# Performance work log

Hardware: AMD Instinct MI355X
Metric: run time of the kernel (lower is better)

The kernel has to match this reference:

```python
import jax, jax.numpy as jnp
import numpy as np

D_MODEL, N_HEAD, D_HEAD, N_LAYERS, D_FF = 1024, 16, 64, 6, 4096
SEQ_LEN, MEM_LEN, BATCH, CLAMP_LEN = 512, 128, 4, 512
LN_EPS = 1e-5


def layernorm(x, g, b):
    mu = jnp.mean(x, axis=-1, keepdims=True)
    var = jnp.var(x, axis=-1, keepdims=True)
    return (x - mu) * jax.lax.rsqrt(var + LN_EPS) * g + b


def rel_shift(x):
    # x: (qlen, rlen, B, H) -> Transformer-XL relative shift
    q, r, b, n = x.shape
    zp = jnp.zeros((q, 1, b, n), x.dtype)
    xp = jnp.concatenate([zp, x], axis=1).reshape(r + 1, q, b, n)
    return xp[1:].reshape(q, r, b, n)


def pos_embedding(klen):
    # sinusoidal embedding on positions klen-1 .. 0, clamped at CLAMP_LEN
    pos = jnp.arange(klen - 1, -1, -1.0, dtype=jnp.float32)
    pos = jnp.minimum(pos, float(CLAMP_LEN))
    inv_freq = 1.0 / (10000.0 ** (jnp.arange(0.0, D_MODEL, 2.0) / D_MODEL))
    sin_inp = pos[:, None] * inv_freq[None, :]  # (klen, D/2)
    return jnp.concatenate([jnp.sin(sin_inp), jnp.cos(sin_inp)], axis=-1)  # (klen, D)


def setup_inputs() -> dict:
    key = jax.random.key(0)
    ks = jax.random.split(key, 16)
    s = 0.02
    return {
        "inputs": jax.random.normal(ks[0], (SEQ_LEN, BATCH, D_MODEL), jnp.float32),
        "mems": jax.random.normal(ks[1], (N_LAYERS, MEM_LEN, BATCH, D_MODEL), jnp.float32),
        "r_w_bias": jax.random.normal(ks[2], (N_HEAD, D_HEAD), jnp.float32) * s,
        "r_r_bias": jax.random.normal(ks[3], (N_HEAD, D_HEAD), jnp.float32) * s,
        "qkv_w": jax.random.normal(ks[4], (N_LAYERS, 3 * N_HEAD * D_HEAD, D_MODEL), jnp.float32) * s,
        "r_w": jax.random.normal(ks[5], (N_LAYERS, N_HEAD * D_HEAD, D_MODEL), jnp.float32) * s,
        "o_w": jax.random.normal(ks[6], (N_LAYERS, D_MODEL, N_HEAD * D_HEAD), jnp.float32) * s,
        "ln1_g": jnp.ones((N_LAYERS, D_MODEL), jnp.float32),
        "ln1_b": jnp.zeros((N_LAYERS, D_MODEL), jnp.float32),
        "ff_w1": jax.random.normal(ks[7], (N_LAYERS, D_FF, D_MODEL), jnp.float32) * s,
        "ff_b1": jnp.zeros((N_LAYERS, D_FF), jnp.float32),
        "ff_w2": jax.random.normal(ks[8], (N_LAYERS, D_MODEL, D_FF), jnp.float32) * s,
        "ff_b2": jnp.zeros((N_LAYERS, D_MODEL), jnp.float32),
        "ln2_g": jnp.ones((N_LAYERS, D_MODEL), jnp.float32),
        "ln2_b": jnp.zeros((N_LAYERS, D_MODEL), jnp.float32),
        "fin_g": jnp.ones((D_MODEL,), jnp.float32),
        "fin_b": jnp.zeros((D_MODEL,), jnp.float32),
    }


def reference(inputs, mems, r_w_bias, r_r_bias, qkv_w, r_w, o_w,
              ln1_g, ln1_b, ff_w1, ff_b1, ff_w2, ff_b2, ln2_g, ln2_b,
              fin_g, fin_b):
    qlen, bsz, _ = inputs.shape
    mlen = mems.shape[1]
    klen = mlen + qlen
    scale = 1.0 / np.sqrt(D_HEAD)

    pos_emb = pos_embedding(klen)  # (klen, D)
    # causal mask with memory: True = masked
    attn_mask = jnp.triu(jnp.ones((qlen, klen), bool), k=1 + mlen)

    x = inputs  # (T, B, D)
    for l in range(N_LAYERS):
        # ---- relative multi-head attention (pre_lnorm) ----
        cat = jnp.concatenate([mems[l], x], axis=0)           # (klen, B, D)
        h = layernorm(cat, ln1_g[l], ln1_b[l])
        w_heads = jnp.einsum('kbd,ed->kbe', h, qkv_w[l])      # (klen, B, 3HD)
        r_head_k = jnp.einsum('kd,ed->ke', pos_emb, r_w[l])   # (klen, HD)
        hd = N_HEAD * D_HEAD
        q = w_heads[-qlen:, :, :hd].reshape(qlen, bsz, N_HEAD, D_HEAD)
        k = w_heads[:, :, hd:2 * hd].reshape(klen, bsz, N_HEAD, D_HEAD)
        v = w_heads[:, :, 2 * hd:].reshape(klen, bsz, N_HEAD, D_HEAD)
        r_head_k = r_head_k.reshape(klen, N_HEAD, D_HEAD)

        AC = jnp.einsum('ibnd,jbnd->ijbn', q + r_w_bias, k)
        BD = rel_shift(jnp.einsum('ibnd,jnd->ijbn', q + r_r_bias, r_head_k))
        score = (AC + BD) * scale                              # (q, k, B, H)
        score = jnp.where(attn_mask[:, :, None, None], -jnp.inf, score)
        prob = jax.nn.softmax(score, axis=1)
        attn_vec = jnp.einsum('ijbn,jbnd->ibnd', prob, v).reshape(qlen, bsz, hd)
        attn_out = jnp.einsum('ibe,de->ibd', attn_vec, o_w[l])
        x = x + attn_out

        # ---- position-wise FFN (pre_lnorm) ----
        hf = layernorm(x, ln2_g[l], ln2_b[l])
        hf = jax.nn.relu(jnp.einsum('ibd,fd->ibf', hf, ff_w1[l]) + ff_b1[l])
        hf = jnp.einsum('ibf,df->ibd', hf, ff_w2[l]) + ff_b2[l]
        x = x + hf

    return layernorm(x, fin_g, fin_b)
```

## Files before the change

### kernel.cpp

```cpp
#include <hip/hip_runtime.h>
#include <math.h>
#include <stdint.h>

#define DM    1024
#define NH    16
#define DH    64
#define NL    6
#define DFF   4096
#define QLEN  512
#define MLEN  128
#define B_    4
#define KL    640
#define CLAMP 512
#define EPS   1e-5f

typedef _Float16 f16x8 __attribute__((ext_vector_type(8)));
typedef _Float16 f16x4 __attribute__((ext_vector_type(4)));
typedef float    f32x4 __attribute__((ext_vector_type(4)));

__device__ __forceinline__ void gload16(const void* g, void* l) {
  __builtin_amdgcn_global_load_lds(
      (const __attribute__((address_space(1))) void*)g,
      (__attribute__((address_space(3))) void*)l, 16, 0, 0);
}

__device__ __forceinline__ float block_sum(float v, float* sm4) {
#pragma unroll
  for (int o = 32; o > 0; o >>= 1) v += __shfl_down(v, o, 64);
  int lane = threadIdx.x & 63, wid = threadIdx.x >> 6;
  if (lane == 0) sm4[wid] = v;
  __syncthreads();
  float r = sm4[0] + sm4[1] + sm4[2] + sm4[3];
  __syncthreads();
  return r;
}

__global__ __launch_bounds__(256) void pos_emb_kernel(_Float16* __restrict__ pe) {
  int p = blockIdx.x;
  float pos = fminf((float)(KL - 1 - p), (float)CLAMP);
  for (int f = threadIdx.x; f < 512; f += 256) {
    float inv = powf(10000.0f, -(float)f * (1.0f / 512.0f));
    float a = pos * inv;
    pe[(size_t)p * DM + f]       = (_Float16)sinf(a);
    pe[(size_t)p * DM + 512 + f] = (_Float16)cosf(a);
  }
}

__global__ __launch_bounds__(256) void cast_all_kernel(
    const float* __restrict__ qkv, const float* __restrict__ rw,
    const float* __restrict__ ow, const float* __restrict__ f1,
    const float* __restrict__ f2,
    _Float16* __restrict__ dq, _Float16* __restrict__ dr,
    _Float16* __restrict__ dow, _Float16* __restrict__ d1,
    _Float16* __restrict__ d2) {
  size_t i = ((size_t)blockIdx.x * 256 + threadIdx.x) * 8;
  const float* s; _Float16* d; size_t off;
  if (i < 18874368)      { s = qkv; d = dq;  off = 0; }
  else if (i < 25165824) { s = rw;  d = dr;  off = 18874368; }
  else if (i < 31457280) { s = ow;  d = dow; off = 25165824; }
  else if (i < 56623104) { s = f1;  d = d1;  off = 31457280; }
  else                   { s = f2;  d = d2;  off = 56623104; }
  size_t k = i - off;
  float4 a = *(const float4*)(s + k);
  float4 b = *(const float4*)(s + k + 4);
  f16x8 o = { (_Float16)a.x, (_Float16)a.y, (_Float16)a.z, (_Float16)a.w,
              (_Float16)b.x, (_Float16)b.y, (_Float16)b.z, (_Float16)b.w };
  *(f16x8*)(d + k) = o;
}

template <int OUTF16>
__global__ __launch_bounds__(256) void ln_kernel(
    const float* __restrict__ src0, const float* __restrict__ src1,
    const float* __restrict__ g, const float* __restrict__ b,
    float* __restrict__ outf, _Float16* __restrict__ outh, int rows0) {
  __shared__ float sm4[4];
  int row = blockIdx.x;
  const float* src = (row < rows0) ? (src0 + (size_t)row * DM)
                                   : (src1 + (size_t)(row - rows0) * DM);
  float4 v = ((const float4*)src)[threadIdx.x];
  float mean = block_sum(v.x + v.y + v.z + v.w, sm4) * (1.0f / DM);
  float dx = v.x - mean, dy = v.y - mean, dz = v.z - mean, dw = v.w - mean;
  float var = block_sum(dx * dx + dy * dy + dz * dz + dw * dw, sm4) * (1.0f / DM);
  float rstd = rsqrtf(var + EPS);
  float4 gg = ((const float4*)g)[threadIdx.x];
  float4 bb = ((const float4*)b)[threadIdx.x];
  float ox = dx * rstd * gg.x + bb.x;
  float oy = dy * rstd * gg.y + bb.y;
  float oz = dz * rstd * gg.z + bb.z;
  float ow = dw * rstd * gg.w + bb.w;
  if (OUTF16) {
    f16x4 o = { (_Float16)ox, (_Float16)oy, (_Float16)oz, (_Float16)ow };
    *(f16x4*)(outh + (size_t)row * DM + threadIdx.x * 4) = o;
  } else {
    float4 o = { ox, oy, oz, ow };
    ((float4*)(outf + (size_t)row * DM))[threadIdx.x] = o;
  }
}

template <int BIAS, int RELU, int RESID, int OUTF16>
__global__ __launch_bounds__(256) void gemm_mfma(
    const _Float16* __restrict__ A, const _Float16* __restrict__ B,
    const float* __restrict__ bias, const float* __restrict__ resid,
    float* __restrict__ Cf, _Float16* __restrict__ Ch,
    int M, int N, int K) {
  __shared__ alignas(16) _Float16 As[128 * 32];
  __shared__ alignas(16) _Float16 Bs[128 * 32];
  const int t = threadIdx.x;
  const int lane = t & 63, wid = t >> 6;
  const int m0 = blockIdx.y * 128, n0 = blockIdx.x * 128;
  const int wm = (wid >> 1) * 64, wn = (wid & 1) * 64;

  const int c0 = wid * 64 + lane, c1 = c0 + 256;
  const _Float16* Ap0 = A + (size_t)(m0 + (c0 >> 2)) * K + (c0 & 3) * 8;
  const _Float16* Ap1 = A + (size_t)(m0 + (c1 >> 2)) * K + (c1 & 3) * 8;
  const _Float16* Bp0 = B + (size_t)(n0 + (c0 >> 2)) * K + (c0 & 3) * 8;
  const _Float16* Bp1 = B + (size_t)(n0 + (c1 >> 2)) * K + (c1 & 3) * 8;
  _Float16* Asw0 = &As[wid * 512];
  _Float16* Asw1 = &As[wid * 512 + 2048];
  _Float16* Bsw0 = &Bs[wid * 512];
  _Float16* Bsw1 = &Bs[wid * 512 + 2048];

  f32x4 acc[4][4] = {};
  for (int k0 = 0; k0 < K; k0 += 32) {
    __syncthreads();
    gload16(Ap0 + k0, Asw0);
    gload16(Ap1 + k0, Asw1);
    gload16(Bp0 + k0, Bsw0);
    gload16(Bp1 + k0, Bsw1);
    __syncthreads();
    f16x8 af[4], bf[4];
#pragma unroll
    for (int f = 0; f < 4; ++f) {
      af[f] = *(const f16x8*)&As[(wm + f * 16 + (lane & 15)) * 32 + (lane >> 4) * 8];
      bf[f] = *(const f16x8*)&Bs[(wn + f * 16 + (lane & 15)) * 32 + (lane >> 4) * 8];
    }
#pragma unroll
    for (int i = 0; i < 4; ++i)
#pragma unroll
      for (int j = 0; j < 4; ++j)
        acc[i][j] = __builtin_amdgcn_mfma_f32_16x16x32_f16(af[i], bf[j], acc[i][j], 0, 0, 0);
  }
#pragma unroll
  for (int i = 0; i < 4; ++i) {
#pragma unroll
    for (int j = 0; j < 4; ++j) {
      const int n = n0 + wn + j * 16 + (lane & 15);
      float bv = 0.0f;
      if (BIAS) bv = bias[n];
#pragma unroll
      for (int r = 0; r < 4; ++r) {
        const int m = m0 + wm + i * 16 + (lane >> 4) * 4 + r;
        float v = acc[i][j][r] + bv;
        if (RELU) v = fmaxf(v, 0.0f);
        if (RESID) v += resid[(size_t)m * N + n];
        if (OUTF16) Ch[(size_t)m * N + n] = (_Float16)v;
        else        Cf[(size_t)m * N + n] = v;
      }
    }
  }
}

__global__ __launch_bounds__(256) void gemm_sk(
    const _Float16* __restrict__ A, const _Float16* __restrict__ B,
    _Float16* __restrict__ pk, int M, int N, int K, int Ks) {
  __shared__ alignas(16) _Float16 As[128 * 32];
  __shared__ alignas(16) _Float16 Bs[128 * 32];
  const int t = threadIdx.x;
  const int lane = t & 63, wid = t >> 6;
  const int m0 = blockIdx.y * 128, n0 = blockIdx.x * 128;
  const int z = blockIdx.z;
  const int kbase = z * Ks;
  const int wm = (wid >> 1) * 64, wn = (wid & 1) * 64;

  const int c0 = wid * 64 + lane, c1 = c0 + 256;
  const _Float16* Ap0 = A + (size_t)(m0 + (c0 >> 2)) * K + kbase + (c0 & 3) * 8;
  const _Float16* Ap1 = A + (size_t)(m0 + (c1 >> 2)) * K + kbase + (c1 & 3) * 8;
  const _Float16* Bp0 = B + (size_t)(n0 + (c0 >> 2)) * K + kbase + (c0 & 3) * 8;
  const _Float16* Bp1 = B + (size_t)(n0 + (c1 >> 2)) * K + kbase + (c1 & 3) * 8;
  _Float16* Asw0 = &As[wid * 512];
  _Float16* Asw1 = &As[wid * 512 + 2048];
  _Float16* Bsw0 = &Bs[wid * 512];
  _Float16* Bsw1 = &Bs[wid * 512 + 2048];

  f32x4 acc[4][4] = {};
  for (int k0 = 0; k0 < Ks; k0 += 32) {
    __syncthreads();
    gload16(Ap0 + k0, Asw0);
    gload16(Ap1 + k0, Asw1);
    gload16(Bp0 + k0, Bsw0);
    gload16(Bp1 + k0, Bsw1);
    __syncthreads();
    f16x8 af[4], bf[4];
#pragma unroll
    for (int f = 0; f < 4; ++f) {
      af[f] = *(const f16x8*)&As[(wm + f * 16 + (lane & 15)) * 32 + (lane >> 4) * 8];
      bf[f] = *(const f16x8*)&Bs[(wn + f * 16 + (lane & 15)) * 32 + (lane >> 4) * 8];
    }
#pragma unroll
    for (int i = 0; i < 4; ++i)
#pragma unroll
      for (int j = 0; j < 4; ++j)
        acc[i][j] = __builtin_amdgcn_mfma_f32_16x16x32_f16(af[i], bf[j], acc[i][j], 0, 0, 0);
  }
  _Float16* out = pk + (size_t)z * M * N;
#pragma unroll
  for (int i = 0; i < 4; ++i)
#pragma unroll
    for (int j = 0; j < 4; ++j) {
      const int n = n0 + wn + j * 16 + (lane & 15);
#pragma unroll
      for (int r = 0; r < 4; ++r) {
        const int m = m0 + wm + i * 16 + (lane >> 4) * 4 + r;
        out[(size_t)m * N + n] = (_Float16)acc[i][j][r];
      }
    }
}

template <int SK, int BIAS, int RELU, int RESID, int OUTF16>
__global__ __launch_bounds__(256) void reduce_k(
    const _Float16* __restrict__ pk, const float* __restrict__ bias,
    const float* __restrict__ resid, float* __restrict__ Cf,
    _Float16* __restrict__ Ch, int MN, int Nmask) {
  const int idx = (blockIdx.x * 256 + threadIdx.x) * 8;
  float s[8] = {};
#pragma unroll
  for (int zz = 0; zz < SK; ++zz) {
    f16x8 v = *(const f16x8*)(pk + (size_t)zz * MN + idx);
#pragma unroll
    for (int e = 0; e < 8; ++e) s[e] += (float)v[e];
  }
  if (BIAS) {
    const int n0 = idx & Nmask;
#pragma unroll
    for (int e = 0; e < 8; ++e) s[e] += bias[n0 + e];
  }
  if (RELU)
#pragma unroll
    for (int e = 0; e < 8; ++e) s[e] = fmaxf(s[e], 0.0f);
  if (RESID) {
    float4 r0 = *(const float4*)(resid + idx);
    float4 r1 = *(const float4*)(resid + idx + 4);
    s[0] += r0.x; s[1] += r0.y; s[2] += r0.z; s[3] += r0.w;
    s[4] += r1.x; s[5] += r1.y; s[6] += r1.z; s[7] += r1.w;
  }
  if (OUTF16) {
    f16x8 o;
#pragma unroll
    for (int e = 0; e < 8; ++e) o[e] = (_Float16)s[e];
    *(f16x8*)(Ch + idx) = o;
  } else {
    float4 o0 = { s[0], s[1], s[2], s[3] };
    float4 o1 = { s[4], s[5], s[6], s[7] };
    *(float4*)(Cf + idx) = o0;
    *(float4*)(Cf + idx + 4) = o1;
  }
}

__global__ __launch_bounds__(256, 3) void attn_kernel(
    const _Float16* __restrict__ wh,
    const _Float16* __restrict__ rk,
    const float* __restrict__ rwb,
    const float* __restrict__ rrb,
    _Float16* __restrict__ po,
    float* __restrict__ pm,
    float* __restrict__ pl) {
  __shared__ alignas(16) _Float16 KS[64 * 72];
  __shared__ alignas(16) _Float16 VT[64 * 72];
  __shared__ alignas(16) _Float16 RR[128 * 72];
  __shared__ alignas(16) _Float16 QS[4][16 * 72];

  const int i0 = blockIdx.x * 64, n = blockIdx.y;
  const int b = blockIdx.z & 3, zz = blockIdx.z >> 2;
  const int t = threadIdx.x, lane = t & 63, wid = t >> 6;
  const int g = lane >> 4, li = lane & 15;
  const int strip = wid * 16;
  _Float16* QSw = QS[wid];

  f16x8 qw[2], qr[2];
#pragma unroll
  for (int ks_ = 0; ks_ < 2; ++ks_) {
    const _Float16* qp =
        wh + ((size_t)(MLEN + i0 + strip + li) * B_ + b) * 3072 + n * 64 + ks_ * 32 + g * 8;
    f16x8 qv = *(const f16x8*)qp;
#pragma unroll
    for (int e = 0; e < 8; ++e) {
      float f0 = (float)qv[e];
      qw[ks_][e] = (_Float16)(f0 + rwb[n * 64 + ks_ * 32 + g * 8 + e]);
      qr[ks_][e] = (_Float16)(f0 + rrb[n * 64 + ks_ * 32 + g * 8 + e]);
    }
  }

  f32x4 o_[4] = {};
  float mrun[4], lrun[4];
#pragma unroll
  for (int r = 0; r < 4; ++r) { mrun[r] = -INFINITY; lrun[r] = 0.0f; }

  const float SC = 0.125f * 1.44269504f;
  const int ntiles = i0 / 64 + 3;
  for (int tt = zz; tt < ntiles; tt += 2) {
    const int j0 = tt * 64;
    __syncthreads();
    {
      int row = t >> 2, c = (t & 3) * 16;
      const _Float16* kp = wh + ((size_t)(j0 + row) * B_ + b) * 3072 + 1024 + n * 64 + c;
      *(f16x8*)&KS[row * 72 + c] = *(const f16x8*)kp;
      *(f16x8*)&KS[row * 72 + c + 8] = *(const f16x8*)(kp + 8);
    }
#pragma unroll
    for (int it = 0; it < 2; ++it) {
      int j = t & 63, d0 = (t >> 6) * 8 + it * 32;
      f16x8 vv = *(const f16x8*)(wh + ((size_t)(j0 + j) * B_ + b) * 3072 + 2048 + n * 64 + d0);
#pragma unroll
      for (int e = 0; e < 8; ++e) VT[(d0 + e) * 72 + j] = vv[e];
    }
    {
      int row = t >> 1, c = (t & 1) * 32;
      int mrow = j0 - i0 + 448 + row;
      if (mrow > KL - 1) mrow = KL - 1;
      const _Float16* rp = rk + (size_t)mrow * 6144 + n * 64 + c;
#pragma unroll
      for (int cc = 0; cc < 32; cc += 8)
        *(f16x8*)&RR[row * 72 + c + cc] = *(const f16x8*)(rp + cc);
    }
    __syncthreads();
    f32x4 acs[4] = {};
#pragma unroll
    for (int ks_ = 0; ks_ < 2; ++ks_)
#pragma unroll
      for (int cf = 0; cf < 4; ++cf) {
        f16x8 bk = *(const f16x8*)&KS[(cf * 16 + li) * 72 + ks_ * 32 + g * 8];
        acs[cf] = __builtin_amdgcn_mfma_f32_16x16x32_f16(qw[ks_], bk, acs[cf], 0, 0, 0);
      }
#pragma unroll
    for (int half = 0; half < 2; ++half) {
      f32x4 acq[4] = {};
#pragma unroll
      for (int ks_ = 0; ks_ < 2; ++ks_)
#pragma unroll
        for (int cf = 0; cf < 4; ++cf) {
          f16x8 br = *(const f16x8*)&RR[((half * 4 + cf) * 16 + li) * 72 + ks_ * 32 + g * 8];
          acq[cf] = __builtin_amdgcn_mfma_f32_16x16x32_f16(qr[ks_], br, acq[cf], 0, 0, 0);
        }
#pragma unroll
      for (int cf = 0; cf < 4; ++cf)
#pragma unroll
        for (int r = 0; r < 4; ++r) {
          int il = strip + g * 4 + r;
          int jl = (half * 4 + cf) * 16 + li - 63 + il;
          if ((unsigned)jl < 64u) QSw[(g * 4 + r) * 72 + jl] = (_Float16)acq[cf][r];
        }
    }
    float pf[4][4], fac[4];
#pragma unroll
    for (int r = 0; r < 4; ++r) {
      int il = strip + g * 4 + r, gi = i0 + il;
      float sv[4], mx = -INFINITY;
#pragma unroll
      for (int cf = 0; cf < 4; ++cf) {
        int jl = cf * 16 + li;
        float v = (acs[cf][r] + (float)QSw[(g * 4 + r) * 72 + jl]) * SC;
        if (j0 + jl > gi + MLEN) v = -INFINITY;
        sv[cf] = v;
        mx = fmaxf(mx, v);
      }
#pragma unroll
      for (int o2 = 1; o2 < 16; o2 <<= 1) mx = fmaxf(mx, __shfl_xor(mx, o2, 64));
      float mnew = fmaxf(mrun[r], mx);
      float fc = exp2f(mrun[r] - mnew);
      float sum = 0.0f;
#pragma unroll
      for (int cf = 0; cf < 4; ++cf) { pf[cf][r] = exp2f(sv[cf] - mnew); sum += pf[cf][r]; }
#pragma unroll
      for (int o2 = 1; o2 < 16; o2 <<= 1) sum += __shfl_xor(sum, o2, 64);
      lrun[r] = lrun[r] * fc + sum;
      mrun[r] = mnew;
      fac[r] = fc;
    }
#pragma unroll
    for (int cf = 0; cf < 4; ++cf)
#pragma unroll
      for (int r = 0; r < 4; ++r)
        QSw[(g * 4 + r) * 72 + cf * 16 + li] = (_Float16)pf[cf][r];
#pragma unroll
    for (int cf = 0; cf < 4; ++cf)
#pragma unroll
      for (int r = 0; r < 4; ++r)
        o_[cf][r] *= fac[r];
#pragma unroll
    for (int ks_ = 0; ks_ < 2; ++ks_) {
      f16x8 pa = *(const f16x8*)&QSw[li * 72 + ks_ * 32 + g * 8];
#pragma unroll
      for (int cf = 0; cf < 4; ++cf) {
        f16x8 bv = *(const f16x8*)&VT[(cf * 16 + li) * 72 + ks_ * 32 + g * 8];
        o_[cf] = __builtin_amdgcn_mfma_f32_16x16x32_f16(pa, bv, o_[cf], 0, 0, 0);
      }
    }
  }
  const size_t obase = (size_t)zz * (QLEN * B_ * 1024);
#pragma unroll
  for (int cf = 0; cf < 4; ++cf)
#pragma unroll
    for (int r = 0; r < 4; ++r) {
      int row = strip + g * 4 + r;
      float l = lrun[r];
      float oo = (l > 0.0f) ? o_[cf][r] / l : 0.0f;
      po[obase + ((size_t)(i0 + row) * B_ + b) * 1024 + n * 64 + cf * 16 + li] = (_Float16)oo;
    }
  if (li == 0) {
#pragma unroll
    for (int r = 0; r < 4; ++r) {
      int row = strip + g * 4 + r;
      int idx = ((i0 + row) * B_ + b) * 16 + n;
      pm[zz * 32768 + idx] = (lrun[r] > 0.0f) ? mrun[r] : -3.0e38f;
      pl[zz * 32768 + idx] = lrun[r];
    }
  }
}

__global__ __launch_bounds__(256) void attn_combine(
    const _Float16* __restrict__ po, const float* __restrict__ pm,
    const float* __restrict__ pl, _Float16* __restrict__ av) {
  const size_t e = ((size_t)blockIdx.x * 256 + threadIdx.x) * 8;
  const int mlidx = (int)(e >> 10) * 16 + (((int)e & 1023) >> 6);
  float m1 = pm[mlidx], m2 = pm[32768 + mlidx];
  float l1 = pl[mlidx], l2 = pl[32768 + mlidx];
  float M = fmaxf(m1, m2);
  float w1 = l1 * exp2f(m1 - M), w2 = l2 * exp2f(m2 - M);
  float inv = 1.0f / (w1 + w2);
  w1 *= inv; w2 *= inv;
  f16x8 o1 = *(const f16x8*)(po + e);
  f16x8 o2 = *(const f16x8*)(po + 2097152 + e);
  f16x8 o;
#pragma unroll
  for (int k = 0; k < 8; ++k) o[k] = (_Float16)(w1 * (float)o1[k] + w2 * (float)o2[k]);
  *(f16x8*)(av + e) = o;
}

extern "C" void kernel_launch(void* const* d_in, const int* in_sizes, int n_in,
                              void* d_out, int out_size, void* d_ws, size_t ws_size,
                              hipStream_t stream) {
  const float* inputs = (const float*)d_in[0];
  const float* mems   = (const float*)d_in[1];
  const float* rwb    = (const float*)d_in[2];
  const float* rrb    = (const float*)d_in[3];
  const float* qkv_w  = (const float*)d_in[4];
  const float* r_w    = (const float*)d_in[5];
  const float* o_w    = (const float*)d_in[6];
  const float* ln1_g  = (const float*)d_in[7];
  const float* ln1_b  = (const float*)d_in[8];
  const float* ff_w1  = (const float*)d_in[9];
  const float* ff_b1  = (const float*)d_in[10];
  const float* ff_w2  = (const float*)d_in[11];
  const float* ff_b2  = (const float*)d_in[12];
  const float* ln2_g  = (const float*)d_in[13];
  const float* ln2_b  = (const float*)d_in[14];
  const float* fin_g  = (const float*)d_in[15];
  const float* fin_b  = (const float*)d_in[16];
  float* out = (float*)d_out;

  float* ws = (float*)d_ws;
  float* xbuf = ws;
  _Float16* fb = (_Float16*)(ws + 2097152);
  _Float16* wh_h   = fb;
  _Float16* rk_all = wh_h + 7864320;
  _Float16* pe_h   = rk_all + 3932160;
  _Float16* h_h    = pe_h + 655360;
  _Float16* av_h   = h_h + 2621440;
  _Float16* ffh_h  = av_h + 2097152;
  _Float16* pk     = ffh_h + 8388608;
  _Float16* po     = pk + 8388608;
  float*    pm     = (float*)(po + 4194304);
  float*    pl     = pm + 65536;
  _Float16* wq_all = (_Float16*)(pl + 65536);
  _Float16* rw_all = wq_all + 18874368;
  _Float16* wo_all = rw_all + 6291456;
  _Float16* w1_all = wo_all + 6291456;
  _Float16* w2_all = w1_all + 25165824;

  pos_emb_kernel<<<KL, 256, 0, stream>>>(pe_h);
  cast_all_kernel<<<39936, 256, 0, stream>>>(
      qkv_w, r_w, o_w, ff_w1, ff_w2, wq_all, rw_all, wo_all, w1_all, w2_all);
  gemm_sk<<<dim3(6144 / 128, 640 / 128, 2), 256, 0, stream>>>(
      pe_h, rw_all, pk, KL, 6144, DM, DM / 2);
  reduce_k<2, 0, 0, 0, 1><<<KL * 6144 / 2048, 256, 0, stream>>>(
      pk, nullptr, nullptr, nullptr, rk_all, KL * 6144, 0);

  const float* xcur = inputs;
  for (int l = 0; l < NL; ++l) {
    ln_kernel<1><<<KL * B_, 256, 0, stream>>>(
        mems + (size_t)l * MLEN * B_ * DM, xcur,
        ln1_g + l * DM, ln1_b + l * DM, nullptr, h_h, MLEN * B_);
    gemm_mfma<0, 0, 0, 1><<<dim3(3072 / 128, 2560 / 128), 256, 0, stream>>>(
        h_h, wq_all + (size_t)l * 3145728, nullptr, nullptr, nullptr, wh_h, 2560, 3072, DM);
    attn_kernel<<<dim3(QLEN / 64, NH, B_ * 2), 256, 0, stream>>>(
        wh_h, rk_all + (size_t)l * 1024, rwb, rrb, po, pm, pl);
    attn_combine<<<1024, 256, 0, stream>>>(po, pm, pl, av_h);
    gemm_sk<<<dim3(DM / 128, (QLEN * B_) / 128, 4), 256, 0, stream>>>(
        av_h, wo_all + (size_t)l * 1048576, pk, QLEN * B_, DM, DM, DM / 4);
    reduce_k<4, 0, 0, 1, 0><<<QLEN * B_ * DM / 2048, 256, 0, stream>>>(
        pk, nullptr, xcur, xbuf, nullptr, QLEN * B_ * DM, DM - 1);
    ln_kernel<1><<<QLEN * B_, 256, 0, stream>>>(
        xbuf, nullptr, ln2_g + l * DM, ln2_b + l * DM, nullptr, h_h, 1 << 30);
    gemm_mfma<1, 1, 0, 1><<<dim3(DFF / 128, (QLEN * B_) / 128), 256, 0, stream>>>(
        h_h, w1_all + (size_t)l * 4194304, ff_b1 + (size_t)l * DFF, nullptr,
        nullptr, ffh_h, QLEN * B_, DFF, DM);
    gemm_sk<<<dim3(DM / 128, (QLEN * B_) / 128, 4), 256, 0, stream>>>(
        ffh_h, w2_all + (size_t)l * 4194304, pk, QLEN * B_, DM, DFF, DFF / 4);
    reduce_k<4, 1, 0, 1, 0><<<QLEN * B_ * DM / 2048, 256, 0, stream>>>(
        pk, ff_b2 + (size_t)l * DM, xbuf, xbuf, nullptr, QLEN * B_ * DM, DM - 1);
    xcur = xbuf;
  }
  ln_kernel<0><<<QLEN * B_, 256, 0, stream>>>(xbuf, nullptr, fin_g, fin_b, out, nullptr, 1 << 30);
}
```

Before: 1.237 ms.

## Fuse fp32-to-fp16 weight conversion into GEMM B-tile loads

After: 1.298 ms. 1.05x slower.

```diff
diff --git a/kernel.cpp b/kernel.cpp
--- a/kernel.cpp
+++ b/kernel.cpp
@@ -44,28 +44,6 @@
     pe[(size_t)p * DM + f]       = (_Float16)sinf(a);
     pe[(size_t)p * DM + 512 + f] = (_Float16)cosf(a);
   }
-}
-
-__global__ __launch_bounds__(256) void cast_all_kernel(
-    const float* __restrict__ qkv, const float* __restrict__ rw,
-    const float* __restrict__ ow, const float* __restrict__ f1,
-    const float* __restrict__ f2,
-    _Float16* __restrict__ dq, _Float16* __restrict__ dr,
-    _Float16* __restrict__ dow, _Float16* __restrict__ d1,
-    _Float16* __restrict__ d2) {
-  size_t i = ((size_t)blockIdx.x * 256 + threadIdx.x) * 8;
-  const float* s; _Float16* d; size_t off;
-  if (i < 18874368)      { s = qkv; d = dq;  off = 0; }
-  else if (i < 25165824) { s = rw;  d = dr;  off = 18874368; }
-  else if (i < 31457280) { s = ow;  d = dow; off = 25165824; }
-  else if (i < 56623104) { s = f1;  d = d1;  off = 31457280; }
-  else                   { s = f2;  d = d2;  off = 56623104; }
-  size_t k = i - off;
-  float4 a = *(const float4*)(s + k);
-  float4 b = *(const float4*)(s + k + 4);
-  f16x8 o = { (_Float16)a.x, (_Float16)a.y, (_Float16)a.z, (_Float16)a.w,
-              (_Float16)b.x, (_Float16)b.y, (_Float16)b.z, (_Float16)b.w };
-  *(f16x8*)(d + k) = o;
 }
 
 template <int OUTF16>
@@ -99,7 +77,7 @@
 
 template <int BIAS, int RELU, int RESID, int OUTF16>
 __global__ __launch_bounds__(256) void gemm_mfma(
-    const _Float16* __restrict__ A, const _Float16* __restrict__ B,
+    const _Float16* __restrict__ A, const float* __restrict__ B,
     const float* __restrict__ bias, const float* __restrict__ resid,
     float* __restrict__ Cf, _Float16* __restrict__ Ch,
     int M, int N, int K) {
@@ -113,20 +91,30 @@
   const int c0 = wid * 64 + lane, c1 = c0 + 256;
   const _Float16* Ap0 = A + (size_t)(m0 + (c0 >> 2)) * K + (c0 & 3) * 8;
   const _Float16* Ap1 = A + (size_t)(m0 + (c1 >> 2)) * K + (c1 & 3) * 8;
-  const _Float16* Bp0 = B + (size_t)(n0 + (c0 >> 2)) * K + (c0 & 3) * 8;
-  const _Float16* Bp1 = B + (size_t)(n0 + (c1 >> 2)) * K + (c1 & 3) * 8;
   _Float16* Asw0 = &As[wid * 512];
   _Float16* Asw1 = &As[wid * 512 + 2048];
-  _Float16* Bsw0 = &Bs[wid * 512];
-  _Float16* Bsw1 = &Bs[wid * 512 + 2048];
+  const float* Bq[4];
+#pragma unroll
+  for (int it = 0; it < 4; ++it) {
+    int ch = it * 256 + t;
+    Bq[it] = B + (size_t)(n0 + (ch >> 3)) * K + (ch & 7) * 4;
+  }
 
   f32x4 acc[4][4] = {};
   for (int k0 = 0; k0 < K; k0 += 32) {
+    float4 bv[4];
+#pragma unroll
+    for (int it = 0; it < 4; ++it) bv[it] = *(const float4*)(Bq[it] + k0);
     __syncthreads();
     gload16(Ap0 + k0, Asw0);
     gload16(Ap1 + k0, Asw1);
-    gload16(Bp0 + k0, Bsw0);
-    gload16(Bp1 + k0, Bsw1);
+#pragma unroll
+    for (int it = 0; it < 4; ++it) {
+      int ch = it * 256 + t;
+      f16x4 hv = { (_Float16)bv[it].x, (_Float16)bv[it].y,
+                   (_Float16)bv[it].z, (_Float16)bv[it].w };
+      *(f16x4*)&Bs[(ch >> 3) * 32 + (ch & 7) * 4] = hv;
+    }
     __syncthreads();
     f16x8 af[4], bf[4];
 #pragma unroll
@@ -161,7 +149,7 @@
 }
 
 __global__ __launch_bounds__(256) void gemm_sk(
-    const _Float16* __restrict__ A, const _Float16* __restrict__ B,
+    const _Float16* __restrict__ A, const float* __restrict__ B,
     _Float16* __restrict__ pk, int M, int N, int K, int Ks) {
   __shared__ alignas(16) _Float16 As[128 * 32];
   __shared__ alignas(16) _Float16 Bs[128 * 32];
@@ -175,20 +163,30 @@
   const int c0 = wid * 64 + lane, c1 = c0 + 256;
   const _Float16* Ap0 = A + (size_t)(m0 + (c0 >> 2)) * K + kbase + (c0 & 3) * 8;
   const _Float16* Ap1 = A + (size_t)(m0 + (c1 >> 2)) * K + kbase + (c1 & 3) * 8;
-  const _Float16* Bp0 = B + (size_t)(n0 + (c0 >> 2)) * K + kbase + (c0 & 3) * 8;
-  const _Float16* Bp1 = B + (size_t)(n0 + (c1 >> 2)) * K + kbase + (c1 & 3) * 8;
   _Float16* Asw0 = &As[wid * 512];
   _Float16* Asw1 = &As[wid * 512 + 2048];
-  _Float16* Bsw0 = &Bs[wid * 512];
-  _Float16* Bsw1 = &Bs[wid * 512 + 2048];
+  const float* Bq[4];
+#pragma unroll
+  for (int it = 0; it < 4; ++it) {
+    int ch = it * 256 + t;
+    Bq[it] = B + (size_t)(n0 + (ch >> 3)) * K + kbase + (ch & 7) * 4;
+  }
 
   f32x4 acc[4][4] = {};
   for (int k0 = 0; k0 < Ks; k0 += 32) {
+    float4 bv[4];
+#pragma unroll
+    for (int it = 0; it < 4; ++it) bv[it] = *(const float4*)(Bq[it] + k0);
     __syncthreads();
     gload16(Ap0 + k0, Asw0);
     gload16(Ap1 + k0, Asw1);
-    gload16(Bp0 + k0, Bsw0);
-    gload16(Bp1 + k0, Bsw1);
+#pragma unroll
+    for (int it = 0; it < 4; ++it) {
+      int ch = it * 256 + t;
+      f16x4 hv = { (_Float16)bv[it].x, (_Float16)bv[it].y,
+                   (_Float16)bv[it].z, (_Float16)bv[it].w };
+      *(f16x4*)&Bs[(ch >> 3) * 32 + (ch & 7) * 4] = hv;
+    }
     __syncthreads();
     f16x8 af[4], bf[4];
 #pragma unroll
@@ -471,17 +469,10 @@
   _Float16* po     = pk + 8388608;
   float*    pm     = (float*)(po + 4194304);
   float*    pl     = pm + 65536;
-  _Float16* wq_all = (_Float16*)(pl + 65536);
-  _Float16* rw_all = wq_all + 18874368;
-  _Float16* wo_all = rw_all + 6291456;
-  _Float16* w1_all = wo_all + 6291456;
-  _Float16* w2_all = w1_all + 25165824;
 
   pos_emb_kernel<<<KL, 256, 0, stream>>>(pe_h);
-  cast_all_kernel<<<39936, 256, 0, stream>>>(
-      qkv_w, r_w, o_w, ff_w1, ff_w2, wq_all, rw_all, wo_all, w1_all, w2_all);
   gemm_sk<<<dim3(6144 / 128, 640 / 128, 2), 256, 0, stream>>>(
-      pe_h, rw_all, pk, KL, 6144, DM, DM / 2);
+      pe_h, r_w, pk, KL, 6144, DM, DM / 2);
   reduce_k<2, 0, 0, 0, 1><<<KL * 6144 / 2048, 256, 0, stream>>>(
       pk, nullptr, nullptr, nullptr, rk_all, KL * 6144, 0);
 
@@ -491,21 +482,21 @@
         mems + (size_t)l * MLEN * B_ * DM, xcur,
         ln1_g + l * DM, ln1_b + l * DM, nullptr, h_h, MLEN * B_);
     gemm_mfma<0, 0, 0, 1><<<dim3(3072 / 128, 2560 / 128), 256, 0, stream>>>(
-        h_h, wq_all + (size_t)l * 3145728, nullptr, nullptr, nullptr, wh_h, 2560, 3072, DM);
+        h_h, qkv_w + (size_t)l * 3145728, nullptr, nullptr, nullptr, wh_h, 2560, 3072, DM);
     attn_kernel<<<dim3(QLEN / 64, NH, B_ * 2), 256, 0, stream>>>(
         wh_h, rk_all + (size_t)l * 1024, rwb, rrb, po, pm, pl);
     attn_combine<<<1024, 256, 0, stream>>>(po, pm, pl, av_h);
     gemm_sk<<<dim3(DM / 128, (QLEN * B_) / 128, 4), 256, 0, stream>>>(
-        av_h, wo_all + (size_t)l * 1048576, pk, QLEN * B_, DM, DM, DM / 4);
+        av_h, o_w + (size_t)l * 1048576, pk, QLEN * B_, DM, DM, DM / 4);
     reduce_k<4, 0, 0, 1, 0><<<QLEN * B_ * DM / 2048, 256, 0, stream>>>(
         pk, nullptr, xcur, xbuf, nullptr, QLEN * B_ * DM, DM - 1);
     ln_kernel<1><<<QLEN * B_, 256, 0, stream>>>(
         xbuf, nullptr, ln2_g + l * DM, ln2_b + l * DM, nullptr, h_h, 1 << 30);
     gemm_mfma<1, 1, 0, 1><<<dim3(DFF / 128, (QLEN * B_) / 128), 256, 0, stream>>>(
-        h_h, w1_all + (size_t)l * 4194304, ff_b1 + (size_t)l * DFF, nullptr,
+        h_h, ff_w1 + (size_t)l * 4194304, ff_b1 + (size_t)l * DFF, nullptr,
         nullptr, ffh_h, QLEN * B_, DFF, DM);
     gemm_sk<<<dim3(DM / 128, (QLEN * B_) / 128, 4), 256, 0, stream>>>(
-        ffh_h, w2_all + (size_t)l * 4194304, pk, QLEN * B_, DM, DFF, DFF / 4);
+        ffh_h, ff_w2 + (size_t)l * 4194304, pk, QLEN * B_, DM, DFF, DFF / 4);
     reduce_k<4, 1, 0, 1, 0><<<QLEN * B_ * DM / 2048, 256, 0, stream>>>(
         pk, ff_b2 + (size_t)l * DM, xbuf, xbuf, nullptr, QLEN * B_ * DM, DM - 1);
     xcur = xbuf;
```
